# Kernel optimization log

Measured on AMD Instinct MI355X. Metric: run time of the kernel, lower is better.

The kernel has to match this reference:

```python
import jax, jax.numpy as jnp
import numpy as np

# Per-task block sizes, sorted descending (powers of 2), as in _InverseLogDetCache
N = (262144, 65536, 16384)
TOTAL = 262144 + 65536 + 16384  # 344064
DIAG_SHIFT = 10.0  # keeps Schur complement S away from 0 (plays role of noise)


def setup_inputs() -> dict:
    key = jax.random.key(0)
    ks = jax.random.split(key, 14)
    rn = lambda k, n: jax.random.normal(k, (n,), dtype=jnp.float32)
    return {
        "lam00_re": rn(ks[0], N[0]) + DIAG_SHIFT,
        "lam00_im": rn(ks[1], N[0]),
        "lam01_re": rn(ks[2], N[0]),
        "lam01_im": rn(ks[3], N[0]),
        "lam02_re": rn(ks[4], N[0]),
        "lam02_im": rn(ks[5], N[0]),
        "lam11_re": rn(ks[6], N[1]) + DIAG_SHIFT,
        "lam11_im": rn(ks[7], N[1]),
        "lam12_re": rn(ks[8], N[1]),
        "lam12_im": rn(ks[9], N[1]),
        "lam22_re": rn(ks[10], N[2]) + DIAG_SHIFT,
        "lam22_im": rn(ks[11], N[2]),
        "z_re": rn(ks[12], TOTAL),
        "z_im": rn(ks[13], TOTAL),
    }


def _step(A, B, lam_ll, n_l):
    """One recursive block Schur-complement update.
    A: (Ra, Ra, na) complex current inverse; B: (Ra*r, n_l) off-diag lam block;
    lam_ll: (n_l,) diagonal lam; returns updated A (R+1, R+1, n_l) and logdet inc."""
    Ra, na = A.shape[0], A.shape[-1]
    r = na // n_l
    Bvec = B.reshape(Ra, -1)                              # (Ra, na)
    T = (Bvec[None, :, :] * A).sum(1).reshape(-1, n_l)    # (R, n_l), R = Ra*r
    M = (B.conj() * T).sum(0)                             # (n_l,)
    S = lam_ll - M                                        # Schur complement diag
    logdet_inc = jnp.log(jnp.abs(S)).sum()
    P = T / S                                             # (R, n_l)
    C = P[:, None, :] * T[None, :, :].conj()              # (R, R, n_l)
    # scatter-add old inverse A into the refined block structure of C
    ii0, ii1, ii2 = jnp.meshgrid(jnp.arange(Ra), jnp.arange(Ra), jnp.arange(na), indexing='ij')
    ii0, ii1, ii2 = ii0.ravel(), ii1.ravel(), ii2.ravel()
    jj0 = ii2 % n_l
    jj1 = ii2 // n_l
    C = C.at[ii0 * r + jj1, ii1 * r + jj1, jj0].add(A.reshape(-1))
    ur = jnp.concatenate([C, -P[:, None, :]], axis=1)                       # (R, R+1, n_l)
    br = jnp.concatenate([-P.conj()[None, :, :], (1.0 / S)[None, None, :]], axis=1)  # (1, R+1, n_l)
    return jnp.concatenate([ur, br], axis=0), logdet_inc


def _forward(lams, z):
    A = (1.0 / lams[(0, 0)])[None, None, :]               # (1, 1, N[0])
    logdet = jnp.log(jnp.abs(lams[(0, 0)])).sum()
    for l in range(1, len(N)):
        B = jnp.concatenate([lams[(k, l)] for k in range(l)], axis=0).reshape(-1, N[l])
        A, inc = _step(A, B, lams[(l, l)], N[l])
        logdet = logdet + inc
    # tilde-to-tilde gram matrix solve: z (TOTAL,) -> (1, R, n_min) * A, sum block rows
    n_min = N[-1]
    zb = z.reshape(1, -1, n_min)                          # (1, 21, n_min)
    zout = (zb * A).sum(-2).reshape(-1)                   # (TOTAL,)
    return A, logdet, zout


def reference(lam00_re, lam00_im, lam01_re, lam01_im, lam02_re, lam02_im,
              lam11_re, lam11_im, lam12_re, lam12_im, lam22_re, lam22_im,
              z_re, z_im):
    lams = {
        (0, 0): lam00_re + 1j * lam00_im,
        (0, 1): lam01_re + 1j * lam01_im,
        (0, 2): lam02_re + 1j * lam02_im,
        (1, 1): lam11_re + 1j * lam11_im,
        (1, 2): lam12_re + 1j * lam12_im,
        (2, 2): lam22_re + 1j * lam22_im,
    }
    z = z_re + 1j * z_im
    A, logdet, zout = _forward(lams, z)
    return (jnp.stack([A.real, A.imag]), logdet, jnp.stack([zout.real, zout.imag]))
```

## Files before the change

### kernel.cpp

```cpp
#include <hip/hip_runtime.h>

#define N2 16384
#define N1 65536

#define OUT_AIM 7225344
#define OUT_LD  14450688
#define OUT_ZRE 14450689
#define OUT_ZIM 14794753

#define L_T2R  0
#define L_T2I  1280
#define L_M2   2560
#define L_SC   3072
#define L_IS2R 9728
#define L_IS2I 9792
#define L_RED  9856
#define L_TOT  9864

#define SC(idx, u, jl) lds[L_SC + (((idx)*4 + (u)) * 64) + (jl)]


#define ST2(addr, v0, v1) do {                                     \
    union { float f[2]; long L; } _u; _u.f[0] = (v0); _u.f[1] = (v1); \
    *(long*)(addr) = _u.L; } while (0)

#define SLOT_PREP(s, P)                                                       \
    const int  p##s    = (P);                                                 \
    const bool is20_##s = (p##s == 20);                                       \
    const int  ap_##s  = p##s >> 2, up_##s = p##s & 3;                        \
    float ppr0_##s=0.f, ppi0_##s=0.f, ppr1_##s=0.f, ppi1_##s=0.f;             \
    float par0_##s=0.f, pai0_##s=0.f, par1_##s=0.f, pai1_##s=0.f;             \
    if (!is20_##s) {                                                          \
        const float tpr0 = lds[L_T2R + p##s*64 + c2], tpr1 = lds[L_T2R + p##s*64 + c2+1]; \
        const float tpi0 = lds[L_T2I + p##s*64 + c2], tpi1 = lds[L_T2I + p##s*64 + c2+1]; \
        ppr0_##s = tpr0*is2r0 - tpi0*is2i0;  ppi0_##s = tpr0*is2i0 + tpi0*is2r0; \
        ppr1_##s = tpr1*is2r1 - tpi1*is2i1;  ppi1_##s = tpr1*is2i1 + tpi1*is2r1; \
        if (ap_##s < 4) {                                                     \
            par0_##s = SC(8+ap_##s,  up_##s, c2);   pai0_##s = SC(12+ap_##s, up_##s, c2);   \
            par1_##s = SC(8+ap_##s,  up_##s, c2+1); pai1_##s = SC(12+ap_##s, up_##s, c2+1); \
        }                                                                     \
    }                                                                         \
    float zar0_##s=0.f, zai0_##s=0.f, zar1_##s=0.f, zai1_##s=0.f;

#define SLOT_Q(s) do {                                                        \
    float ar0, ai0, ar1, ai1;                                                 \
    if (is20_##s) {                                                           \
        if (q < 20) {                                                         \
            ar0 = -(tr0*is2r0 - ti0*is2i0);  ai0 = tr0*is2i0 + ti0*is2r0;     \
            ar1 = -(tr1*is2r1 - ti1*is2i1);  ai1 = tr1*is2i1 + ti1*is2r1;     \
        } else { ar0=is2r0; ai0=is2i0; ar1=is2r1; ai1=is2i1; }                \
    } else if (q < 20) {                                                      \
        ar0 = ppr0_##s*tr0 + ppi0_##s*ti0;  ai0 = ppi0_##s*tr0 - ppr0_##s*ti0;\
        ar1 = ppr1_##s*tr1 + ppi1_##s*ti1;  ai1 = ppi1_##s*tr1 - ppr1_##s*ti1;\
        if ((q & 3) == up_##s) {                  \
            const int b = q >> 2;                                             \
            if (ap_##s < 4) {                                                 \
                if (b < 4) {                                                  \
                    const float tbr0 = SC(b, up_##s, c2),   tbi0 = SC(4+b, up_##s, c2);   \
                    const float tbr1 = SC(b, up_##s, c2+1), tbi1 = SC(4+b, up_##s, c2+1); \
                    ar0 += par0_##s*tbr0 + pai0_##s*tbi0;  ai0 += pai0_##s*tbr0 - par0_##s*tbi0; \
                    ar1 += par1_##s*tbr1 + pai1_##s*tbi1;  ai1 += pai1_##s*tbr1 - par1_##s*tbi1; \
                    if (b == ap_##s) {                         \
                        ar0 += SC(16+ap_##s, up_##s, c2);   ai0 += SC(20+ap_##s, up_##s, c2);   \
                        ar1 += SC(16+ap_##s, up_##s, c2+1); ai1 += SC(20+ap_##s, up_##s, c2+1); \
                    }                                                         \
                } else { ar0 -= par0_##s; ai0 -= pai0_##s; ar1 -= par1_##s; ai1 -= pai1_##s; } \
            } else {                                                          \
                if (b < 4) {                                \
                    ar0 -= SC(8+b, up_##s, c2);   ai0 += SC(12+b, up_##s, c2);   \
                    ar1 -= SC(8+b, up_##s, c2+1); ai1 += SC(12+b, up_##s, c2+1); \
                } else {                                            \
                    ar0 += SC(24, up_##s, c2);   ai0 += SC(25, up_##s, c2);   \
                    ar1 += SC(24, up_##s, c2+1); ai1 += SC(25, up_##s, c2+1); \
                }                                                             \
            }                                                                 \
        }                                                                     \
    } else { ar0 = -ppr0_##s; ai0 = -ppi0_##s; ar1 = -ppr1_##s; ai1 = -ppi1_##s; } \
    ST2(out + (p##s*21+q)*N2 + j2,           ar0, ar1);                       \
    ST2(out + OUT_AIM + (p##s*21+q)*N2 + j2, ai0, ai1);                       \
    zar0_##s += zr2.x*ar0 - zi2.x*ai0;  zai0_##s += zr2.x*ai0 + zi2.x*ar0;    \
    zar1_##s += zr2.y*ar1 - zi2.y*ai1;  zai1_##s += zr2.y*ai1 + zi2.y*ar1;    \
} while (0)

#define SLOT_ZSTORE(s) do {                                                   \
    float a0 = zar0_##s, b0 = zai0_##s, a1 = zar1_##s, b1 = zai1_##s;         \
    a0 += __shfl_xor(a0, 32, 64);  b0 += __shfl_xor(b0, 32, 64);              \
    a1 += __shfl_xor(a1, 32, 64);  b1 += __shfl_xor(b1, 32, 64);              \
    const int src = l >> 1;                                                   \
    const float e_r = __shfl(a0, src, 64), o_r = __shfl(a1, src, 64);         \
    const float e_i = __shfl(b0, src, 64), o_i = __shfl(b1, src, 64);         \
    const float zvr = (l & 1) ? o_r : e_r;                                    \
    const float zvi = (l & 1) ? o_i : e_i;                                    \
    out[OUT_ZRE + p##s*N2 + j0 + l] = zvr;                                    \
    out[OUT_ZIM + p##s*N2 + j0 + l] = zvi;                                    \
} while (0)

__global__ __launch_bounds__(448) void fused_kernel(
    const float* __restrict__ l00r, const float* __restrict__ l00i,
    const float* __restrict__ l01r, const float* __restrict__ l01i,
    const float* __restrict__ l02r, const float* __restrict__ l02i,
    const float* __restrict__ l11r, const float* __restrict__ l11i,
    const float* __restrict__ l12r, const float* __restrict__ l12i,
    const float* __restrict__ l22r, const float* __restrict__ l22i,
    const float* __restrict__ zre,  const float* __restrict__ zim,
    float* __restrict__ out, double* __restrict__ ld_partial)
{
    __shared__ float lds[L_TOT];
    const int t   = threadIdx.x;
    const int jl  = t & 63;
    const int j0  = blockIdx.x * 64;
    float ld = 0.f;

    if (t < 256) {
        const int u = t >> 6;
        const int m = u * N2 + (j0 + jl);

        float i0r[4], i0i[4], t1r[4], t1i[4], p1r[4], p1i[4];
        float m1r = 0.f, m1i = 0.f;
#pragma unroll
        for (int k = 0; k < 4; ++k) {
            const int i = k * N1 + m;
            const float ar = l00r[i], ai = l00i[i];
            const float br = l01r[i], bi = l01i[i];
            const float d  = ar*ar + ai*ai;
            const float rd = 1.f / d;
            ld += 0.5f * logf(d);
            const float xr = ar * rd, xi = -ai * rd;
            i0r[k] = xr; i0i[k] = xi;
            const float tr = br*xr - bi*xi;
            const float ti = br*xi + bi*xr;
            t1r[k] = tr; t1i[k] = ti;
            m1r += br*tr + bi*ti;
            m1i += br*ti - bi*tr;
        }
        const float s1r = l11r[m] - m1r;
        const float s1i = l11i[m] - m1i;
        const float ds1 = s1r*s1r + s1i*s1i;
        ld += 0.5f * logf(ds1);
        const float rds1 = 1.f / ds1;
        const float is1r = s1r * rds1, is1i = -s1i * rds1;
#pragma unroll
        for (int k = 0; k < 4; ++k) {
            p1r[k] = t1r[k]*is1r - t1i[k]*is1i;
            p1i[k] = t1r[k]*is1i + t1i[k]*is1r;
        }

        float bcr[5], bci[5];
#pragma unroll
        for (int a = 0; a < 4; ++a) { bcr[a] = l02r[a*N1+m]; bci[a] = l02i[a*N1+m]; }
        bcr[4] = l12r[m]; bci[4] = l12i[m];

        float wr = -bcr[4], wi = -bci[4];
#pragma unroll
        for (int b = 0; b < 4; ++b) {
            wr += bcr[b]*t1r[b] + bci[b]*t1i[b];
            wi += bci[b]*t1r[b] - bcr[b]*t1i[b];
        }
        float ur[5], ui[5];
#pragma unroll
        for (int a = 0; a < 4; ++a) {
            ur[a] = p1r[a]*wr - p1i[a]*wi + bcr[a]*i0r[a] - bci[a]*i0i[a];
            ui[a] = p1r[a]*wi + p1i[a]*wr + bcr[a]*i0i[a] + bci[a]*i0r[a];
        }
        {
            float vr = bcr[4]*is1r - bci[4]*is1i;
            float vi = bcr[4]*is1i + bci[4]*is1r;
#pragma unroll
            for (int b = 0; b < 4; ++b) {
                vr -= bcr[b]*p1r[b] + bci[b]*p1i[b];
                vi -= bci[b]*p1r[b] - bcr[b]*p1i[b];
            }
            ur[4] = vr; ui[4] = vi;
        }
        float m2r = 0.f, m2i = 0.f;
#pragma unroll
        for (int a = 0; a < 5; ++a) {
            lds[L_T2R + (a*4+u)*64 + jl] = ur[a];
            lds[L_T2I + (a*4+u)*64 + jl] = ui[a];
            m2r += bcr[a]*ur[a] + bci[a]*ui[a];
            m2i += bcr[a]*ui[a] - bci[a]*ur[a];
        }
        lds[L_M2 + (0*4+u)*64 + jl] = m2r;
        lds[L_M2 + (1*4+u)*64 + jl] = m2i;
#pragma unroll
        for (int b = 0; b < 4; ++b) {
            SC(b,      u, jl) = t1r[b];  SC(4+b,  u, jl) = t1i[b];
            SC(8+b,    u, jl) = p1r[b];  SC(12+b, u, jl) = p1i[b];
            SC(16+b,   u, jl) = i0r[b];  SC(20+b, u, jl) = i0i[b];
        }
        SC(24, u, jl) = is1r;  SC(25, u, jl) = is1i;
    }
    __syncthreads();

    if (t < 64) {
        float s2r = l22r[j0 + t], s2i = l22i[j0 + t];
#pragma unroll
        for (int u = 0; u < 4; ++u) {
            s2r -= lds[L_M2 + (0*4+u)*64 + t];
            s2i -= lds[L_M2 + (1*4+u)*64 + t];
        }
        const float ds2  = s2r*s2r + s2i*s2i;
        const float rds2 = 1.f / ds2;
        lds[L_IS2R + t] =  s2r * rds2;
        lds[L_IS2I + t] = -s2i * rds2;
        ld += 0.5f * logf(ds2);
    }
    __syncthreads();

    const int g  = t >> 6;
    const int l  = t & 63;
    const int h  = l >> 5;
    const int c  = l & 31;
    const int c2 = 2*c;
    const int j2 = j0 + c2;

    const float is2r0 = lds[L_IS2R + c2],   is2r1 = lds[L_IS2R + c2+1];
    const float is2i0 = lds[L_IS2I + c2],   is2i1 = lds[L_IS2I + c2+1];

    SLOT_PREP(0, g)
    SLOT_PREP(1, g + 7)
    SLOT_PREP(2, g + 14)

#pragma unroll
    for (int qi = 0; qi < 11; ++qi) {
        const int q = 2*qi + h;
        if (q >= 21) continue;
        float tr0=0.f, tr1=0.f, ti0=0.f, ti1=0.f;
        if (q < 20) {
            tr0 = lds[L_T2R + q*64 + c2];  tr1 = lds[L_T2R + q*64 + c2+1];
            ti0 = lds[L_T2I + q*64 + c2];  ti1 = lds[L_T2I + q*64 + c2+1];
        }
        const float2 zr2 = *(const float2*)(zre + q*N2 + j2);
        const float2 zi2 = *(const float2*)(zim + q*N2 + j2);
        SLOT_Q(0);
        SLOT_Q(1);
        SLOT_Q(2);
    }

    SLOT_ZSTORE(0);
    SLOT_ZSTORE(1);
    SLOT_ZSTORE(2);

    {
        float v = ld;
#pragma unroll
        for (int off = 32; off > 0; off >>= 1) v += __shfl_down(v, off, 64);
        __syncthreads();
        if (jl == 0) lds[L_RED + g] = v;
        __syncthreads();
        if (t == 0) {
            double s = 0.0;
#pragma unroll
            for (int w = 0; w < 7; ++w) s += (double)lds[L_RED + w];
            ld_partial[blockIdx.x] = s;
        }
    }
}

__global__ __launch_bounds__(256) void finalize_kernel(
    const double* __restrict__ part, float* __restrict__ out)
{
    double v = part[threadIdx.x];
#pragma unroll
    for (int off = 32; off > 0; off >>= 1) v += __shfl_down(v, off, 64);
    __shared__ double wsum[4];
    if ((threadIdx.x & 63) == 0) wsum[threadIdx.x >> 6] = v;
    __syncthreads();
    if (threadIdx.x == 0)
        out[OUT_LD] = (float)(wsum[0] + wsum[1] + wsum[2] + wsum[3]);
}

extern "C" void kernel_launch(void* const* d_in, const int* in_sizes, int n_in,
                              void* d_out, int out_size, void* d_ws, size_t ws_size,
                              hipStream_t stream)
{
    const float* l00r = (const float*)d_in[0];
    const float* l00i = (const float*)d_in[1];
    const float* l01r = (const float*)d_in[2];
    const float* l01i = (const float*)d_in[3];
    const float* l02r = (const float*)d_in[4];
    const float* l02i = (const float*)d_in[5];
    const float* l11r = (const float*)d_in[6];
    const float* l11i = (const float*)d_in[7];
    const float* l12r = (const float*)d_in[8];
    const float* l12i = (const float*)d_in[9];
    const float* l22r = (const float*)d_in[10];
    const float* l22i = (const float*)d_in[11];
    const float* zre  = (const float*)d_in[12];
    const float* zim  = (const float*)d_in[13];
    float*  out        = (float*)d_out;
    double* ld_partial = (double*)d_ws;

    fused_kernel<<<dim3(N2/64, 1), dim3(448), 0, stream>>>(
        l00r,l00i,l01r,l01i,l02r,l02i,l11r,l11i,l12r,l12i,l22r,l22i,
        zre,zim, out, ld_partial);
    finalize_kernel<<<1, 256, 0, stream>>>(ld_partial, out);
}
```

Before: 111.1 us.

## Stage A output in block-contiguous workspace then transpose-copy to output

The fused kernel now writes each block's A tile (882 rows of 64 floats) contiguously into a workspace instead of strided 8-byte stores across 441 output rows. A new copy kernel with 882 blocks reads these tiles with float4 loads and writes full contiguous output rows, and also folds in the logdet finalize reduction. The aim is better write coalescing and DRAM locality, paid for with an extra round trip of about 58 MB through the workspace.

```diff
diff --git a/kernel.cpp b/kernel.cpp
--- a/kernel.cpp
+++ b/kernel.cpp
@@ -19,6 +19,8 @@
 
 #define SC(idx, u, jl) lds[L_SC + (((idx)*4 + (u)) * 64) + (jl)]
 
+#define WS_A      0
+#define WS_FLOATS 14450688
 
 #define ST2(addr, v0, v1) do {                                     \
     union { float f[2]; long L; } _u; _u.f[0] = (v0); _u.f[1] = (v1); \
@@ -76,8 +78,8 @@
             }                                                                 \
         }                                                                     \
     } else { ar0 = -ppr0_##s; ai0 = -ppi0_##s; ar1 = -ppr1_##s; ai1 = -ppi1_##s; } \
-    ST2(out + (p##s*21+q)*N2 + j2,           ar0, ar1);                       \
-    ST2(out + OUT_AIM + (p##s*21+q)*N2 + j2, ai0, ai1);                       \
+    ST2(wsA + wsbase + (p##s*21+q)*64 + c2,         ar0, ar1);                \
+    ST2(wsA + wsbase + (441 + p##s*21+q)*64 + c2,   ai0, ai1);                \
     zar0_##s += zr2.x*ar0 - zi2.x*ai0;  zai0_##s += zr2.x*ai0 + zi2.x*ar0;    \
     zar1_##s += zr2.y*ar1 - zi2.y*ai1;  zai1_##s += zr2.y*ai1 + zi2.y*ar1;    \
 } while (0)
@@ -103,12 +105,14 @@
     const float* __restrict__ l12r, const float* __restrict__ l12i,
     const float* __restrict__ l22r, const float* __restrict__ l22i,
     const float* __restrict__ zre,  const float* __restrict__ zim,
-    float* __restrict__ out, double* __restrict__ ld_partial)
+    float* __restrict__ wsA, float* __restrict__ out,
+    double* __restrict__ ld_partial)
 {
     __shared__ float lds[L_TOT];
     const int t   = threadIdx.x;
     const int jl  = t & 63;
     const int j0  = blockIdx.x * 64;
+    const int wsbase = blockIdx.x * 882 * 64;
     float ld = 0.f;
 
     if (t < 256) {
@@ -230,8 +234,8 @@
             tr0 = lds[L_T2R + q*64 + c2];  tr1 = lds[L_T2R + q*64 + c2+1];
             ti0 = lds[L_T2I + q*64 + c2];  ti1 = lds[L_T2I + q*64 + c2+1];
         }
-        const float2 zr2 = *(const float2*)(zre + q*N2 + j2);
-        const float2 zi2 = *(const float2*)(zim + q*N2 + j2);
+        const float2 zr2 = *reinterpret_cast<const float2*>(zre + q*N2 + j2);
+        const float2 zi2 = *reinterpret_cast<const float2*>(zim + q*N2 + j2);
         SLOT_Q(0);
         SLOT_Q(1);
         SLOT_Q(2);
@@ -257,17 +261,35 @@
     }
 }
 
-__global__ __launch_bounds__(256) void finalize_kernel(
-    const double* __restrict__ part, float* __restrict__ out)
+__global__ __launch_bounds__(256) void copy_kernel(
+    const float* __restrict__ ws, const double* __restrict__ ld_partial,
+    float* __restrict__ out)
 {
-    double v = part[threadIdx.x];
-#pragma unroll
-    for (int off = 32; off > 0; off >>= 1) v += __shfl_down(v, off, 64);
-    __shared__ double wsum[4];
-    if ((threadIdx.x & 63) == 0) wsum[threadIdx.x >> 6] = v;
-    __syncthreads();
-    if (threadIdx.x == 0)
-        out[OUT_LD] = (float)(wsum[0] + wsum[1] + wsum[2] + wsum[3]);
+    const int r = blockIdx.x;
+    const int t = threadIdx.x;
+    const size_t rowbase = (r < 441)
+        ? (size_t)r * N2
+        : (size_t)OUT_AIM + (size_t)(r - 441) * N2;
+    const int sub = t >> 4;
+    const int cg  = (t & 15) * 4;
+#pragma unroll
+    for (int it = 0; it < 16; ++it) {
+        const int jt = it * 16 + sub;
+        const float4 v = *reinterpret_cast<const float4*>(
+            ws + ((size_t)jt * 882 + r) * 64 + cg);
+        *reinterpret_cast<float4*>(out + rowbase + jt * 64 + cg) = v;
+    }
+
+    if (r == 0) {
+        __shared__ double wsum[4];
+        double v = ld_partial[t];
+#pragma unroll
+        for (int off = 32; off > 0; off >>= 1) v += __shfl_down(v, off, 64);
+        if ((t & 63) == 0) wsum[t >> 6] = v;
+        __syncthreads();
+        if (t == 0)
+            out[OUT_LD] = (float)(wsum[0] + wsum[1] + wsum[2] + wsum[3]);
+    }
 }
 
 extern "C" void kernel_launch(void* const* d_in, const int* in_sizes, int n_in,
@@ -288,11 +310,12 @@
     const float* l22i = (const float*)d_in[11];
     const float* zre  = (const float*)d_in[12];
     const float* zim  = (const float*)d_in[13];
-    float*  out        = (float*)d_out;
-    double* ld_partial = (double*)d_ws;
+    float*  out = (float*)d_out;
+    float*  wsf = (float*)d_ws;
+    double* ldp = (double*)(wsf + WS_FLOATS);
 
     fused_kernel<<<dim3(N2/64, 1), dim3(448), 0, stream>>>(
         l00r,l00i,l01r,l01i,l02r,l02i,l11r,l11i,l12r,l12i,l22r,l22i,
-        zre,zim, out, ld_partial);
-    finalize_kernel<<<1, 256, 0, stream>>>(ld_partial, out);
+        zre,zim, wsf, out, ldp);
+    copy_kernel<<<dim3(882), dim3(256), 0, stream>>>(wsf, ldp, out);
 }
```

New measurement: 127.0 us. 14.4% more time.
